# Optimization experiments

Hardware: AMD Instinct MI355X
Metric: run time of the kernel (lower is better)

## Reference

```python
import jax, jax.numpy as jnp
import numpy as np

MIN_SIGMA = 0.1
MAX_SIGMA = 10.0


def setup_inputs() -> dict:
    key = jax.random.key(0)
    k1, k2, k3 = jax.random.split(key, 3)
    M, P = 4096, 2
    B, N = 8, 2048
    z = jax.random.normal(k1, (M, P), dtype=jnp.float32)
    mu = jax.random.normal(k2, (B, N, P), dtype=jnp.float32)
    sigma = jax.random.uniform(k3, (B, N, 1), dtype=jnp.float32)
    return {"z": z, "mu": mu, "sigma": sigma}


def reference(z, mu, sigma):
    # z: [M, P] grid points; mu: [B, N, P] token positions; sigma: [B, N, 1]
    sig = jnp.clip(sigma, MIN_SIGMA, MAX_SIGMA)  # [B, N, 1]
    # ||z - mu||^2 via matmul decomposition (avoids [B,N,M,P] intermediate)
    z_sq = jnp.sum(z * z, axis=-1)              # [M]
    mu_sq = jnp.sum(mu * mu, axis=-1, keepdims=True)  # [B, N, 1]
    cross = jnp.einsum("bnp,mp->bnm", mu, z)    # [B, N, M]
    d2 = jnp.maximum(mu_sq + z_sq[None, None, :] - 2.0 * cross, 0.0)  # [B, N, M]
    return jnp.exp(-d2 / (2.0 * sig * sig))     # [B, N, M]
```

## Files before the change

### kernel.cpp

```cpp
#include <hip/hip_runtime.h>
#include <hip/hip_bf16.h>


#define MIN_SIGMA 0.1f
#define MAX_SIGMA 10.0f
#define LOG2E 1.44269504088896340736f

typedef float vf4 __attribute__((ext_vector_type(4)));

constexpr int ROWS_PER_BLOCK = 16;
constexpr int COLS_PER_BLOCK = 1024;

__global__ __launch_bounds__(256) void rbf_v2(
    const float4* __restrict__ z4,
    const float2* __restrict__ mu2,
    const float* __restrict__ sigma,
    float* __restrict__ out,
    int M) {
  const int col0 = blockIdx.x * COLS_PER_BLOCK + threadIdx.x * 4;
  const int bn0 = blockIdx.y * ROWS_PER_BLOCK;

  const float4 za = z4[col0 >> 1];
  const float4 zb = z4[(col0 >> 1) + 1];
  const float zx0 = za.x, zy0 = za.y;
  const float zx1 = za.z, zy1 = za.w;
  const float zx2 = zb.x, zy2 = zb.y;
  const float zx3 = zb.z, zy3 = zb.w;

  float* orow = out + (size_t)bn0 * (size_t)M + col0;

#pragma unroll
  for (int r = 0; r < ROWS_PER_BLOCK; ++r) {
    const int bn = bn0 + r;
    const float2 m = mu2[bn];
    float sg = sigma[bn];
    sg = fminf(fmaxf(sg, MIN_SIGMA), MAX_SIGMA);
    const float c = LOG2E / (2.0f * sg * sg);

    vf4 v;
    {
      const float dx = zx0 - m.x, dy = zy0 - m.y;
      v.x = __builtin_amdgcn_exp2f(-(dx * dx + dy * dy) * c);
    }
    {
      const float dx = zx1 - m.x, dy = zy1 - m.y;
      v.y = __builtin_amdgcn_exp2f(-(dx * dx + dy * dy) * c);
    }
    {
      const float dx = zx2 - m.x, dy = zy2 - m.y;
      v.z = __builtin_amdgcn_exp2f(-(dx * dx + dy * dy) * c);
    }
    {
      const float dx = zx3 - m.x, dy = zy3 - m.y;
      v.w = __builtin_amdgcn_exp2f(-(dx * dx + dy * dy) * c);
    }
    __builtin_nontemporal_store(v, reinterpret_cast<vf4*>(orow));
    orow += M;
  }
}

extern "C" void kernel_launch(void* const* d_in, const int* in_sizes, int n_in,
                              void* d_out, int out_size, void* d_ws,
                              size_t ws_size, hipStream_t stream) {
  const float* z = (const float*)d_in[0];
  const float* mu = (const float*)d_in[1];
  const float* sigma = (const float*)d_in[2];
  float* out = (float*)d_out;

  const int M = in_sizes[0] / 2;
  const int BN = in_sizes[1] / 2;

  dim3 grid(M / COLS_PER_BLOCK, BN / ROWS_PER_BLOCK);
  rbf_v2<<<grid, dim3(256), 0, stream>>>(
      reinterpret_cast<const float4*>(z),
      reinterpret_cast<const float2*>(mu), sigma, out, M);
}
```

Before: 272.6 us.

## Assign one output row per block with regular stores and hardcoded width

Restructures the grid so each block handles one (b,n) row across all 4096 columns, loading mu and sigma once per block and reading z per iteration instead of per row. Nontemporal stores become ordinary stores, and the division is replaced with a hardware reciprocal. Hardcoding M=4096 removes generality, and reloading z (32KB, cached) per block adds L2 traffic. The output write of 268MB dominates, so the store path change is the main lever.

```diff
diff --git a/kernel.cpp b/kernel.cpp
--- a/kernel.cpp
+++ b/kernel.cpp
@@ -8,54 +8,44 @@
 
 typedef float vf4 __attribute__((ext_vector_type(4)));
 
-constexpr int ROWS_PER_BLOCK = 16;
-constexpr int COLS_PER_BLOCK = 1024;
-
-__global__ __launch_bounds__(256) void rbf_v2(
+__global__ __launch_bounds__(256) void rbf_v3(
     const float4* __restrict__ z4,
     const float2* __restrict__ mu2,
     const float* __restrict__ sigma,
-    float* __restrict__ out,
-    int M) {
-  const int col0 = blockIdx.x * COLS_PER_BLOCK + threadIdx.x * 4;
-  const int bn0 = blockIdx.y * ROWS_PER_BLOCK;
+    float* __restrict__ out) {
+  const int bn = blockIdx.x;
 
-  const float4 za = z4[col0 >> 1];
-  const float4 zb = z4[(col0 >> 1) + 1];
-  const float zx0 = za.x, zy0 = za.y;
-  const float zx1 = za.z, zy1 = za.w;
-  const float zx2 = zb.x, zy2 = zb.y;
-  const float zx3 = zb.z, zy3 = zb.w;
+  const float2 m = mu2[bn];
+  float sg = sigma[bn];
+  sg = fminf(fmaxf(sg, MIN_SIGMA), MAX_SIGMA);
+  const float c = (0.5f * LOG2E) * __builtin_amdgcn_rcpf(sg * sg);
 
-  float* orow = out + (size_t)bn0 * (size_t)M + col0;
+  const int t = threadIdx.x;
+  float4* orow = reinterpret_cast<float4*>(out + (size_t)bn * 4096);
 
 #pragma unroll
-  for (int r = 0; r < ROWS_PER_BLOCK; ++r) {
-    const int bn = bn0 + r;
-    const float2 m = mu2[bn];
-    float sg = sigma[bn];
-    sg = fminf(fmaxf(sg, MIN_SIGMA), MAX_SIGMA);
-    const float c = LOG2E / (2.0f * sg * sg);
-
+  for (int j = 0; j < 4; ++j) {
+    const int col4 = t + j * 256;
+    const float4 za = z4[2 * col4];
+    const float4 zb = z4[2 * col4 + 1];
     vf4 v;
     {
-      const float dx = zx0 - m.x, dy = zy0 - m.y;
+      const float dx = za.x - m.x, dy = za.y - m.y;
       v.x = __builtin_amdgcn_exp2f(-(dx * dx + dy * dy) * c);
     }
     {
-      const float dx = zx1 - m.x, dy = zy1 - m.y;
+      const float dx = za.z - m.x, dy = za.w - m.y;
       v.y = __builtin_amdgcn_exp2f(-(dx * dx + dy * dy) * c);
     }
     {
-      const float dx = zx2 - m.x, dy = zy2 - m.y;
+      const float dx = zb.x - m.x, dy = zb.y - m.y;
       v.z = __builtin_amdgcn_exp2f(-(dx * dx + dy * dy) * c);
     }
     {
-      const float dx = zx3 - m.x, dy = zy3 - m.y;
+      const float dx = zb.z - m.x, dy = zb.w - m.y;
       v.w = __builtin_amdgcn_exp2f(-(dx * dx + dy * dy) * c);
     }
-    __builtin_nontemporal_store(v, reinterpret_cast<vf4*>(orow));
-    orow += M;
+    orow[col4] = *reinterpret_cast<float4*>(&v);
   }
 }
 
@@ -67,11 +57,9 @@
   const float* sigma = (const float*)d_in[2];
   float* out = (float*)d_out;
 
-  const int M = in_sizes[0] / 2;
   const int BN = in_sizes[1] / 2;
 
-  dim3 grid(M / COLS_PER_BLOCK, BN / ROWS_PER_BLOCK);
-  rbf_v2<<<grid, dim3(256), 0, stream>>>(
+  rbf_v3<<<dim3(BN), dim3(256), 0, stream>>>(
       reinterpret_cast<const float4*>(z),
-      reinterpret_cast<const float2*>(mu), sigma, out, M);
+      reinterpret_cast<const float2*>(mu), sigma, out);
 }
```

Measured after the change: 256.2 us. 1.06x faster.
